# Kernel tuning notes

Hardware: AMD Instinct MI355X
Metric: run time of the kernel (lower is better)

The kernel has to match this reference:

```python
import jax, jax.numpy as jnp
from jax import lax
import numpy as np

B, H, W, C = 2, 128, 128, 256
HEADS, DH = 8, 32
HD = HEADS * DH  # must equal C (pos_emb reshape constraint)


def _lrelu(t):
    return jnp.where(t > 0, t, 0.01 * t)


def _mlp(t, w1, b1, w2):
    # Linear(dim->hd, bias) -> LeakyReLU -> Linear(hd->hd, no bias)
    return _lrelu(t @ w1.T + b1) @ w2.T


def _dwconv(t, w, b):
    # depthwise 3x3, padding 1; t: NCHW, w: (C,1,3,3)
    o = lax.conv_general_dilated(t, w, (1, 1), ((1, 1), (1, 1)),
                                 dimension_numbers=('NCHW', 'OIHW', 'NCHW'),
                                 feature_group_count=t.shape[1])
    return o + b[None, :, None, None]


def setup_inputs():
    key = jax.random.key(0)
    ks = iter(jax.random.split(key, 48))
    def nrm(shape, s=0.02):
        return jax.random.normal(next(ks), shape, jnp.float32) * s
    inp = {
        'x_in': jax.random.normal(next(ks), (B, H, W, C), jnp.float32),
        'y_in': jax.random.normal(next(ks), (B, H, W, C), jnp.float32),
        # fusion_x / fusion_y: two 1x1 convs (stored as (out,in) matrices)
        'fx_w1': nrm((C, 2 * C)), 'fx_b1': jnp.zeros((C,), jnp.float32),
        'fx_w2': nrm((C, C)),     'fx_b2': jnp.zeros((C,), jnp.float32),
        'fy_w1': nrm((C, 2 * C)), 'fy_b1': jnp.zeros((C,), jnp.float32),
        'fy_w2': nrm((C, C)),     'fy_b2': jnp.zeros((C,), jnp.float32),
        # to_q / to_k / to_v: Linear(C->HD,+b) -> LeakyReLU -> Linear(HD->HD, no b)
        'q_w1': nrm((HD, C)), 'q_b1': jnp.zeros((HD,), jnp.float32), 'q_w2': nrm((HD, HD)),
        'k_w1': nrm((HD, C)), 'k_b1': jnp.zeros((HD,), jnp.float32), 'k_w2': nrm((HD, HD)),
        'v_w1': nrm((HD, C)), 'v_b1': jnp.zeros((HD,), jnp.float32), 'v_w2': nrm((HD, HD)),
        'rescale_x': jnp.ones((HEADS, 1, 1), jnp.float32),
        'rescale_y': jnp.ones((HEADS, 1, 1), jnp.float32),
        'px_w': nrm((C, HD)), 'px_b': jnp.zeros((C,), jnp.float32),
        'py_w': nrm((C, HD)), 'py_b': jnp.zeros((C,), jnp.float32),
        # pos_emb: two depthwise 3x3 convs with GELU between
        'pe_w1': nrm((C, 1, 3, 3)), 'pe_b1': jnp.zeros((C,), jnp.float32),
        'pe_w2': nrm((C, 1, 3, 3)), 'pe_b2': jnp.zeros((C,), jnp.float32),
    }
    return inp


def reference(x_in, y_in, fx_w1, fx_b1, fx_w2, fx_b2, fy_w1, fy_b1, fy_w2, fy_b2,
              q_w1, q_b1, q_w2, k_w1, k_b1, k_w2, v_w1, v_b1, v_w2,
              rescale_x, rescale_y, px_w, px_b, py_w, py_b,
              pe_w1, pe_b1, pe_w2, pe_b2):
    b, h, w, c = x_in.shape
    n = h * w

    xy = jnp.concatenate([x_in, y_in], axis=-1)  # (b,h,w,2c)
    fk_x = _lrelu(jnp.einsum('bhwi,oi->bhwo', xy, fx_w1) + fx_b1)
    fk_x = (jnp.einsum('bhwi,oi->bhwo', fk_x, fx_w2) + fx_b2).reshape(b, n, c)
    fk_y = _lrelu(jnp.einsum('bhwi,oi->bhwo', xy, fy_w1) + fy_b1)
    fk_y = (jnp.einsum('bhwi,oi->bhwo', fk_y, fy_w2) + fy_b2).reshape(b, n, c)

    x = x_in.reshape(b, n, c)
    y = y_in.reshape(b, n, c)
    q_inp_x = _mlp(x, q_w1, q_b1, q_w2)
    k_inp_x = _mlp(fk_x, k_w1, k_b1, k_w2)
    v_inp_x = _mlp(x, v_w1, v_b1, v_w2)
    q_inp_y = _mlp(y, q_w1, q_b1, q_w2)
    k_inp_y = _mlp(fk_y, k_w1, k_b1, k_w2)
    v_inp_y = _mlp(y, v_w1, v_b1, v_w2)

    def split_heads(t):  # (b,n,hd) -> (b,heads,d,n)  (already transposed)
        return t.reshape(b, n, HEADS, DH).transpose(0, 2, 3, 1)

    def l2n(t):
        return t / jnp.maximum(jnp.linalg.norm(t, axis=-1, keepdims=True), 1e-12)

    q_x, k_x, v_x = split_heads(q_inp_x), split_heads(k_inp_x), split_heads(v_inp_x)
    q_y, k_y, v_y = split_heads(q_inp_y), split_heads(k_inp_y), split_heads(v_inp_y)
    q_x, k_x, q_y, k_y = l2n(q_x), l2n(k_x), l2n(q_y), l2n(k_y)

    def pos_emb(v_inp):
        t = v_inp.reshape(b, h, w, c).transpose(0, 3, 1, 2)  # NCHW
        t = _dwconv(t, pe_w1, pe_b1)
        t = jax.nn.gelu(t, approximate=False)
        t = _dwconv(t, pe_w2, pe_b2)
        return t.transpose(0, 2, 3, 1)  # NHWC

    # channel (transposed) cross-attention: d x d maps per head
    attn_x = jax.nn.softmax(jnp.einsum('bhdn,bhen->bhde', k_y, q_x) * rescale_x, axis=-1)
    xo = jnp.einsum('bhde,bhen->bhdn', attn_x, v_x).transpose(0, 3, 1, 2).reshape(b, n, HD)
    out_x = (xo @ px_w.T + px_b).reshape(b, h, w, c) + pos_emb(v_inp_x)

    attn_y = jax.nn.softmax(jnp.einsum('bhdn,bhen->bhde', k_x, q_y) * rescale_y, axis=-1)
    yo = jnp.einsum('bhde,bhen->bhdn', attn_y, v_y).transpose(0, 3, 1, 2).reshape(b, n, HD)
    out_y = (yo @ py_w.T + py_b).reshape(b, h, w, c) + pos_emb(v_inp_y)

    return out_x, out_y
```

## Files before the change

### kernel.cpp

```cpp
#include <hip/hip_runtime.h>
#include <hip/hip_bf16.h>

typedef __hip_bfloat16 bf16;
typedef __attribute__((ext_vector_type(8))) short short8;
typedef __attribute__((ext_vector_type(4))) float f32x4;

static __device__ __forceinline__ float bfbits2f(short s) {
    return __uint_as_float(((unsigned int)(unsigned short)s) << 16);
}
static __device__ __forceinline__ bf16 f2bf(float v) { return __float2bfloat16(v); }
static __device__ __forceinline__ short f2bfbits(float f) {
    bf16 h = __float2bfloat16(f);
    return *reinterpret_cast<short*>(&h);
}

struct PrepArgs {
    const float *x, *y; bf16 *xb, *yb;
    const float* wsrc[10]; bf16* wdst[10]; int wblk[10];
    const float *pw1, *pw2; float *t1, *t2;
    float4* zero;
};

__launch_bounds__(256)
__global__ void prep_kernel(PrepArgs a)
{
    int blk = blockIdx.x, tid = threadIdx.x;
    if (blk < 8192) {
        int t = blk * 256 + tid;
        int which = t >> 20;
        size_t i = (size_t)(t & 1048575) * 8;
        const float4* s = (const float4*)((which ? a.y : a.x) + i);
        float4 u = s[0], v = s[1];
        short8 p;
        p[0] = f2bfbits(u.x); p[1] = f2bfbits(u.y); p[2] = f2bfbits(u.z); p[3] = f2bfbits(u.w);
        p[4] = f2bfbits(v.x); p[5] = f2bfbits(v.y); p[6] = f2bfbits(v.z); p[7] = f2bfbits(v.w);
        *(short8*)((which ? a.yb : a.xb) + i) = p;
    } else if (blk < 8960) {
        int b = blk - 8192;
        int ai = 0, base = 0;
        while (ai < 9 && b >= base + a.wblk[ai]) { base += a.wblk[ai]; ++ai; }
        size_t i = ((size_t)(b - base) * 256 + tid) * 4;
        const float4 v = *(const float4*)(a.wsrc[ai] + i);
        bf16* d = a.wdst[ai] + i;
        d[0] = f2bf(v.x); d[1] = f2bf(v.y); d[2] = f2bf(v.z); d[3] = f2bf(v.w);
    } else if (blk < 8978) {
        int t = (blk - 8960) * 256 + tid;
        if (t < 4608) {
            int which = t >= 2304;
            int i = which ? t - 2304 : t;
            int c = i / 9, k = i % 9;
            (which ? a.t2 : a.t1)[k * 256 + c] = (which ? a.pw2 : a.pw1)[i];
        }
    } else {
        int i = (blk - 8978) * 256 + tid;
        a.zero[i] = make_float4(0.f, 0.f, 0.f, 0.f);
    }
}

template<int ROWS>
static __device__ __forceinline__ void stage8(const bf16* __restrict__ g, int ldk,
                                              char* dst, int tid, long r0, int k0)
{
#pragma unroll
    for (int r = 0; r < ROWS / 128; ++r) {
        int row = r * 128 + (tid >> 2);
        int q = (tid & 3) * 16;
        int srcq = q ^ (((row >> 1) & 3) << 4);
        const char* gsrc = (const char*)(g + (size_t)(r0 + row) * ldk + k0) + srcq;
        char* ldst = dst + r * 8192 + ((tid >> 6) << 10);
        __builtin_amdgcn_global_load_lds(
            (const __attribute__((address_space(1))) unsigned int*)gsrc,
            (__attribute__((address_space(3))) unsigned int*)ldst, 16, 0, 0);
    }
}

static __device__ __forceinline__ int h_off2(int r, int c)
{
    return r * 512 + ((c * 2) ^ ((r & 7) << 4));
}

struct MlpArgs {
    const bf16* B1[2]; const float* b1[2];
    const bf16* W2[2]; const float* b2[2];
    bf16* outb[2]; bf16* outT[2]; float* nrm[2];
};

template<int K1, bool CONCAT, bool B2OUT, bool TRANS0>
__launch_bounds__(512, 4)
__global__ void mlp_kernel(const bf16* __restrict__ A0, const bf16* __restrict__ A1,
                           MlpArgs args)
{
    __shared__ __align__(16) char lds[66560];
    int tid = threadIdx.x;
    int lane = tid & 63, wid = tid >> 6;
    int c16 = lane & 15, kg = lane >> 4;
    int wr = wid >> 2, wc = wid & 3;
    int sel = blockIdx.x;
    long m0 = (long)blockIdx.y * 128;
    const bf16* B1p = args.B1[sel];
    const bf16* W2p = args.W2[sel];
    char* Abuf = lds;
    char* Bbuf = lds + 16384;

    f32x4 acc[4][4];
#pragma unroll
    for (int i = 0; i < 4; ++i)
#pragma unroll
        for (int j = 0; j < 4; ++j) acc[i][j] = (f32x4){0.f, 0.f, 0.f, 0.f};

    stage8<128>(A0, 256, Abuf, tid, m0, 0);
    stage8<256>(B1p, K1, Bbuf, tid, 0, 0);

    int kb = kg * 16;
    int offa[4], offb[4];
#pragma unroll
    for (int mi = 0; mi < 4; ++mi) {
        int row = wr * 64 + mi * 16 + c16;
        offa[mi] = row * 64 + (kb ^ (((row >> 1) & 3) << 4));
    }
#pragma unroll
    for (int ni = 0; ni < 4; ++ni) {
        int row = wc * 64 + ni * 16 + c16;
        offb[ni] = row * 64 + (kb ^ (((row >> 1) & 3) << 4));
    }

    constexpr int NT1 = K1 / 32;
#pragma unroll
    for (int kt = 0; kt < NT1; ++kt) {
        __syncthreads();
        int cur = kt & 1;
        if (kt + 1 < NT1) {
            int k0 = (kt + 1) * 32;
            const bf16* As = A0; int kk = k0;
            if (CONCAT && k0 >= 256) { As = A1; kk = k0 - 256; }
            stage8<128>(As, 256, Abuf + (cur ^ 1) * 8192, tid, m0, kk);
            stage8<256>(B1p, K1, Bbuf + (cur ^ 1) * 16384, tid, 0, k0);
        }
        const char* As = Abuf + cur * 8192;
        const char* Bs = Bbuf + cur * 16384;
        short8 af[4], bfr[4];
#pragma unroll
        for (int mi = 0; mi < 4; ++mi) af[mi] = *(const short8*)(As + offa[mi]);
#pragma unroll
        for (int ni = 0; ni < 4; ++ni) bfr[ni] = *(const short8*)(Bs + offb[ni]);
#pragma unroll
        for (int mi = 0; mi < 4; ++mi)
#pragma unroll
            for (int ni = 0; ni < 4; ++ni)
                acc[mi][ni] = __builtin_amdgcn_mfma_f32_16x16x32_bf16(af[mi], bfr[ni], acc[mi][ni], 0, 0, 0);
    }

    int co0 = wid * 32 + c16;
    short8 wf[2][2];
    wf[0][0] = *(const short8*)(W2p + (size_t)co0 * 256 + kg * 8);
    wf[0][1] = *(const short8*)(W2p + (size_t)(co0 + 16) * 256 + kg * 8);

    float bv1[4];
#pragma unroll
    for (int ni = 0; ni < 4; ++ni) bv1[ni] = args.b1[sel][wc * 64 + ni * 16 + c16];
    __syncthreads();
#pragma unroll
    for (int mi = 0; mi < 4; ++mi)
#pragma unroll
        for (int ni = 0; ni < 4; ++ni) {
            int c = wc * 64 + ni * 16 + c16;
#pragma unroll
            for (int j = 0; j < 4; ++j) {
                int r = wr * 64 + mi * 16 + kg * 4 + j;
                float v = acc[mi][ni][j] + bv1[ni];
                v = v > 0.f ? v : 0.01f * v;
                *(bf16*)(lds + h_off2(r, c)) = f2bf(v);
            }
        }
    __syncthreads();

    f32x4 acc2[8][2];
#pragma unroll
    for (int i = 0; i < 8; ++i) {
        acc2[i][0] = (f32x4){0.f, 0.f, 0.f, 0.f};
        acc2[i][1] = (f32x4){0.f, 0.f, 0.f, 0.f};
    }
#pragma unroll
    for (int kc = 0; kc < 8; ++kc) {
        if (kc < 7) {
            wf[(kc + 1) & 1][0] = *(const short8*)(W2p + (size_t)co0 * 256 + (kc + 1) * 32 + kg * 8);
            wf[(kc + 1) & 1][1] = *(const short8*)(W2p + (size_t)(co0 + 16) * 256 + (kc + 1) * 32 + kg * 8);
        }
#pragma unroll
        for (int mi = 0; mi < 8; ++mi) {
            short8 a2 = *(const short8*)(lds + h_off2(mi * 16 + c16, kc * 32 + kg * 8));
            acc2[mi][0] = __builtin_amdgcn_mfma_f32_16x16x32_bf16(a2, wf[kc & 1][0], acc2[mi][0], 0, 0, 0);
            acc2[mi][1] = __builtin_amdgcn_mfma_f32_16x16x32_bf16(a2, wf[kc & 1][1], acc2[mi][1], 0, 0, 0);
        }
    }

    bool trans = TRANS0 && (sel == 0);
    float vsq[2] = {0.f, 0.f};
    __syncthreads();
    if (trans) {
#pragma unroll
        for (int mi = 0; mi < 8; ++mi)
#pragma unroll
            for (int j2 = 0; j2 < 2; ++j2) {
                int col = co0 + j2 * 16;
#pragma unroll
                for (int j = 0; j < 4; ++j) {
                    float v = acc2[mi][j2][j];
                    vsq[j2] += v * v;
                    int row = mi * 16 + kg * 4 + j;
                    *(bf16*)(lds + col * 256 + ((row * 2) ^ ((col & 7) << 4))) = f2bf(v);
                }
            }
    } else {
        const float* b2p = args.b2[sel];
        float bvo[2];
        bvo[0] = B2OUT ? b2p[co0] : 0.f;
        bvo[1] = B2OUT ? b2p[co0 + 16] : 0.f;
#pragma unroll
        for (int mi = 0; mi < 8; ++mi)
#pragma unroll
            for (int j2 = 0; j2 < 2; ++j2) {
                int col = co0 + j2 * 16;
#pragma unroll
                for (int j = 0; j < 4; ++j) {
                    int row = mi * 16 + kg * 4 + j;
                    *(bf16*)(lds + h_off2(row, col)) = f2bf(acc2[mi][j2][j] + bvo[j2]);
                }
            }
    }
    __syncthreads();
    if (trans) {
        bf16* dst = args.outT[sel];
#pragma unroll
        for (int i = 0; i < 8; ++i) {
            int g = i * 512 + tid;
            int col = g >> 4, rc = g & 15;
            short8 vv = *(const short8*)(lds + col * 256 + ((rc ^ (col & 7)) << 4));
            *(short8*)(dst + (size_t)col * 65536 + m0 + rc * 8) = vv;
        }
        float* cs = (float*)(lds + 65536);
        if (tid < 256) cs[tid] = 0.f;
        __syncthreads();
        atomicAdd(&cs[co0], vsq[0]);
        atomicAdd(&cs[co0 + 16], vsq[1]);
        __syncthreads();
        if (tid < 256)
            atomicAdd(args.nrm[sel] + (int)(m0 >> 14) * 256 + tid, cs[tid]);
    } else {
        bf16* dst = args.outb[sel];
#pragma unroll
        for (int i = 0; i < 8; ++i) {
            int g = i * 512 + tid;
            int row = g >> 5, cc = g & 31;
            short8 vv = *(const short8*)(lds + row * 512 + ((cc ^ (row & 7)) << 4));
            *(short8*)(dst + (size_t)(m0 + row) * 256 + cc * 8) = vv;
        }
    }
}

__launch_bounds__(512, 2)
__global__ void projconv_kernel(const bf16* __restrict__ vbuf, const bf16* __restrict__ PW,
                                const bf16* __restrict__ ctmp,
                                const float* __restrict__ px_b, const float* __restrict__ py_b,
                                const float* __restrict__ peT2, const float* __restrict__ pe_b2,
                                float* __restrict__ outf)
{
    __shared__ __align__(16) char lds[76800];
    float* ldsF = (float*)lds;
    float* ldsW = (float*)(lds + 66560);
    float* ldsB = (float*)(lds + 75776);
    int tid = threadIdx.x;
    int lane = tid & 63, wid = tid >> 6;
    int c16 = lane & 15, kg = lane >> 4;
    int wr = wid >> 2, wc = wid & 3;
    long m0 = (long)blockIdx.y * 128;
    int quarter = (int)(m0 >> 14);
    int y = (int)((m0 & 16383) >> 7);
    char* Abuf = lds;
    char* Bbuf = lds + 16384;

    f32x4 acc[4][4];
#pragma unroll
    for (int i = 0; i < 4; ++i)
#pragma unroll
        for (int j = 0; j < 4; ++j) acc[i][j] = (f32x4){0.f, 0.f, 0.f, 0.f};

    const bf16* Bq = PW + (size_t)quarter * 65536;

    stage8<128>(vbuf, 256, Abuf, tid, m0, 0);
    stage8<256>(Bq, 256, Bbuf, tid, 0, 0);

#pragma unroll
    for (int i = 0; i < 5; ++i) {
        int idx = i * 512 + tid;
        if (idx < 2304) ldsW[idx] = peT2[idx];
    }
    if (tid < 256) ldsB[tid] = (quarter < 2 ? px_b : py_b)[tid] + pe_b2[tid];

    int kb = kg * 16;
    int offa[4], offb[4];
#pragma unroll
    for (int mi = 0; mi < 4; ++mi) {
        int row = wr * 64 + mi * 16 + c16;
        offa[mi] = row * 64 + (kb ^ (((row >> 1) & 3) << 4));
    }
#pragma unroll
    for (int ni = 0; ni < 4; ++ni) {
        int row = wc * 64 + ni * 16 + c16;
        offb[ni] = row * 64 + (kb ^ (((row >> 1) & 3) << 4));
    }

#pragma unroll
    for (int kt = 0; kt < 8; ++kt) {
        __syncthreads();
        int cur = kt & 1;
        if (kt + 1 < 8) {
            int k0 = (kt + 1) * 32;
            stage8<128>(vbuf, 256, Abuf + (cur ^ 1) * 8192, tid, m0, k0);
            stage8<256>(Bq, 256, Bbuf + (cur ^ 1) * 16384, tid, 0, k0);
        }
        const char* As = Abuf + cur * 8192;
        const char* Bs = Bbuf + cur * 16384;
        short8 af[4], bfr[4];
#pragma unroll
        for (int mi = 0; mi < 4; ++mi) af[mi] = *(const short8*)(As + offa[mi]);
#pragma unroll
        for (int ni = 0; ni < 4; ++ni) bfr[ni] = *(const short8*)(Bs + offb[ni]);
#pragma unroll
        for (int mi = 0; mi < 4; ++mi)
#pragma unroll
            for (int ni = 0; ni < 4; ++ni)
                acc[mi][ni] = __builtin_amdgcn_mfma_f32_16x16x32_bf16(af[mi], bfr[ni], acc[mi][ni], 0, 0, 0);
    }

    const bf16* cbase = ctmp + (((size_t)quarter << 14) << 8);
#pragma unroll
    for (int hh = 0; hh < 2; ++hh) {
        __syncthreads();
        if (wr == hh) {
#pragma unroll
            for (int mi = 0; mi < 4; ++mi)
#pragma unroll
                for (int ni = 0; ni < 4; ++ni) {
                    int col = wc * 64 + ni * 16 + c16;
#pragma unroll
                    for (int j = 0; j < 4; ++j)
                        ldsF[(mi * 16 + kg * 4 + j) * 260 + col] = acc[mi][ni][j];
                }
        }
        __syncthreads();
#pragma unroll
        for (int pass = 0; pass < 4; ++pass) {
            int idx = pass * 512 + tid;
            int cg = idx & 31, c0 = cg * 8;
            int xl = idx >> 5;
            int x = hh * 64 + xl;
            float a8[8];
#pragma unroll
            for (int j = 0; j < 8; ++j) a8[j] = ldsB[c0 + j];
#pragma unroll
            for (int dy = -1; dy <= 1; ++dy) {
                int yy = y + dy;
                if (yy < 0 || yy > 127) continue;
#pragma unroll
                for (int dx = -1; dx <= 1; ++dx) {
                    int xx = x + dx;
                    if (xx < 0 || xx > 127) continue;
                    short8 v = *(const short8*)(cbase + (size_t)((yy << 7) + xx) * 256 + c0);
                    const float* wt = ldsW + ((dy + 1) * 3 + dx + 1) * 256 + c0;
#pragma unroll
                    for (int j = 0; j < 8; ++j) a8[j] += wt[j] * bfbits2f(v[j]);
                }
            }
            const float* pf = ldsF + xl * 260 + c0;
#pragma unroll
            for (int j = 0; j < 8; ++j) a8[j] += pf[j];
            float4 o0 = make_float4(a8[0], a8[1], a8[2], a8[3]);
            float4 o1 = make_float4(a8[4], a8[5], a8[6], a8[7]);
            float4* op = (float4*)(outf + (size_t)(m0 + x) * 256 + c0);
            op[0] = o0; op[1] = o1;
        }
    }
}

__launch_bounds__(256)
__global__ void convgram_kernel(const bf16* __restrict__ in, const float* __restrict__ wT,
                                const float* __restrict__ bias, bf16* __restrict__ outb,
                                const bf16* __restrict__ qT, const bf16* __restrict__ kT,
                                float* __restrict__ gram)
{
    __shared__ float g[1024];
    int blk = blockIdx.x, tid = threadIdx.x;
    if (blk < 2048) {
        int t = blk * 256 + tid;
        int cg = t & 31;
        int x = (t >> 5) & 127;
        int chunk = (t >> 12) & 31;
        int img = t >> 17;
        int c0 = cg * 8;

        float w[9][8];
#pragma unroll
        for (int k = 0; k < 9; ++k) {
            float4 a = *(const float4*)(wT + k * 256 + c0);
            float4 bq = *(const float4*)(wT + k * 256 + c0 + 4);
            w[k][0] = a.x; w[k][1] = a.y; w[k][2] = a.z; w[k][3] = a.w;
            w[k][4] = bq.x; w[k][5] = bq.y; w[k][6] = bq.z; w[k][7] = bq.w;
        }
        float bs[8];
        {
            float4 a = *(const float4*)(bias + c0);
            float4 bq = *(const float4*)(bias + c0 + 4);
            bs[0] = a.x; bs[1] = a.y; bs[2] = a.z; bs[3] = a.w;
            bs[4] = bq.x; bs[5] = bq.y; bs[6] = bq.z; bs[7] = bq.w;
        }
        const short8 z = (short8){0, 0, 0, 0, 0, 0, 0, 0};
        bool xm = x > 0, xp = x < 127;
        int y0 = chunk * 4;

        for (int yi = 0; yi < 4; ++yi) {
            int y = y0 + yi;
            float acc[8];
#pragma unroll
            for (int j = 0; j < 8; ++j) acc[j] = bs[j];
#pragma unroll
            for (int ky = -1; ky <= 1; ++ky) {
                int yy = y + ky;
                if (yy < 0 || yy > 127) continue;
                const bf16* rp = in + ((((size_t)img << 14) + (yy << 7) + x) << 8) + c0;
                short8 vm = xm ? *(const short8*)(rp - 256) : z;
                short8 vc = *(const short8*)(rp);
                short8 vp = xp ? *(const short8*)(rp + 256) : z;
                int k0 = (ky + 1) * 3;
#pragma unroll
                for (int j = 0; j < 8; ++j) {
                    acc[j] += w[k0 + 0][j] * bfbits2f(vm[j]);
                    acc[j] += w[k0 + 1][j] * bfbits2f(vc[j]);
                    acc[j] += w[k0 + 2][j] * bfbits2f(vp[j]);
                }
            }
            size_t base = ((((size_t)img << 14) + (y << 7) + x) << 8) + c0;
            short8 p;
#pragma unroll
            for (int j = 0; j < 8; ++j) {
                float a = acc[j];
                a = 0.5f * a * (1.0f + erff(a * 0.70710678118654752f));
                p[j] = f2bfbits(a);
            }
            *(short8*)(outb + base) = p;
        }
    } else {
        int bid = blk - 2048;
        int ns = bid & 15, h = (bid >> 4) & 7, b = (bid >> 7) & 1, pair = bid >> 8;
        int lane = tid & 63, w = tid >> 6;
        long krow = pair ? (long)b * 16384 : (long)(32768 + b * 16384);
        long qrow = pair ? (long)(32768 + b * 16384) : (long)b * 16384;
        long nb = (long)ns * 1024 + w * 256 + (lane >> 4) * 8;
        const bf16* Kp = kT + krow + nb;
        const bf16* Qp = qT + qrow + nb;
        int ch = h * 32 + (lane & 15);

        f32x4 acc[2][2];
#pragma unroll
        for (int i = 0; i < 2; ++i)
#pragma unroll
            for (int j = 0; j < 2; ++j) acc[i][j] = (f32x4){0.f, 0.f, 0.f, 0.f};

        for (int it = 0; it < 8; ++it) {
            short8 af[2], bfr[2];
#pragma unroll
            for (int mi = 0; mi < 2; ++mi)
                af[mi] = *(const short8*)(Kp + (size_t)(ch + mi * 16) * 65536 + it * 32);
#pragma unroll
            for (int ni = 0; ni < 2; ++ni)
                bfr[ni] = *(const short8*)(Qp + (size_t)(ch + ni * 16) * 65536 + it * 32);
#pragma unroll
            for (int mi = 0; mi < 2; ++mi)
#pragma unroll
                for (int ni = 0; ni < 2; ++ni)
                    acc[mi][ni] = __builtin_amdgcn_mfma_f32_16x16x32_bf16(af[mi], bfr[ni], acc[mi][ni], 0, 0, 0);
        }

#pragma unroll
        for (int k = 0; k < 4; ++k) g[tid + k * 256] = 0.f;
        __syncthreads();
#pragma unroll
        for (int mi = 0; mi < 2; ++mi)
#pragma unroll
            for (int ni = 0; ni < 2; ++ni) {
                int e = ni * 16 + (lane & 15);
#pragma unroll
                for (int j = 0; j < 4; ++j) {
                    int d = mi * 16 + (lane >> 4) * 4 + j;
                    atomicAdd(&g[d * 32 + e], acc[mi][ni][j]);
                }
            }
        __syncthreads();
        float* gp = gram + ((size_t)((pair * 2 + b) * 8 + h)) * 1024;
#pragma unroll
        for (int k = 0; k < 4; ++k)
            atomicAdd(gp + tid + k * 256, g[tid + k * 256]);
    }
}

__launch_bounds__(256)
__global__ void attn_pw_kernel(const float* __restrict__ gram, const float* __restrict__ norm2,
                               const float* __restrict__ rsx, const float* __restrict__ rsy,
                               const float* __restrict__ pxw, const float* __restrict__ pyw,
                               bf16* __restrict__ PW)
{
    int bid = blockIdx.x;
    int h = bid & 7, b = (bid >> 3) & 1, pair = bid >> 4;
    const float* G = gram + ((size_t)((pair * 2 + b) * 8 + h)) * 1024;
    const float* nk2 = norm2 + (pair ? (4 + b) : (6 + b)) * 256 + h * 32;
    const float* nq2 = norm2 + (pair ? (2 + b) : (0 + b)) * 256 + h * 32;
    float rs = (pair ? rsy : rsx)[h];
    __shared__ float attn[32][32];
    int t = threadIdx.x;
    if (t < 32) {
        int d = t;
        float nk = fmaxf(sqrtf(nk2[d]), 1e-12f);
        float row[32];
        float mx = -3.4e38f;
#pragma unroll
        for (int e = 0; e < 32; ++e) {
            float nq = fmaxf(sqrtf(nq2[e]), 1e-12f);
            float L = G[d * 32 + e] / (nk * nq) * rs;
            row[e] = L;
            mx = fmaxf(mx, L);
        }
        float sum = 0.f;
#pragma unroll
        for (int e = 0; e < 32; ++e) { row[e] = expf(row[e] - mx); sum += row[e]; }
        float inv = 1.0f / sum;
#pragma unroll
        for (int e = 0; e < 32; ++e) attn[d][e] = row[e] * inv;
    }
    __syncthreads();
    const float* pw = pair ? pyw : pxw;
    int o = t;
    float wrow[32];
#pragma unroll
    for (int d2 = 0; d2 < 32; ++d2) wrow[d2] = pw[o * 256 + h * 32 + d2];
    bf16* dst = PW + ((size_t)(pair * 2 + b) * 256 + o) * 256 + h * 32;
#pragma unroll
    for (int e = 0; e < 32; ++e) {
        float sv = 0.f;
#pragma unroll
        for (int d2 = 0; d2 < 32; ++d2) sv += wrow[d2] * attn[d2][e];
        dst[e] = f2bf(sv);
    }
}

extern "C" void kernel_launch(void* const* d_in, const int* in_sizes, int n_in,
                              void* d_out, int out_size, void* d_ws, size_t ws_size,
                              hipStream_t stream)
{
    const float* x_in  = (const float*)d_in[0];
    const float* y_in  = (const float*)d_in[1];
    const float* fx_w1 = (const float*)d_in[2];
    const float* fx_b1 = (const float*)d_in[3];
    const float* fx_w2 = (const float*)d_in[4];
    const float* fx_b2 = (const float*)d_in[5];
    const float* fy_w1 = (const float*)d_in[6];
    const float* fy_b1 = (const float*)d_in[7];
    const float* fy_w2 = (const float*)d_in[8];
    const float* fy_b2 = (const float*)d_in[9];
    const float* q_w1  = (const float*)d_in[10];
    const float* q_b1  = (const float*)d_in[11];
    const float* q_w2  = (const float*)d_in[12];
    const float* k_w1  = (const float*)d_in[13];
    const float* k_b1  = (const float*)d_in[14];
    const float* k_w2  = (const float*)d_in[15];
    const float* v_w1  = (const float*)d_in[16];
    const float* v_b1  = (const float*)d_in[17];
    const float* v_w2  = (const float*)d_in[18];
    const float* rescale_x = (const float*)d_in[19];
    const float* rescale_y = (const float*)d_in[20];
    const float* px_w  = (const float*)d_in[21];
    const float* px_b  = (const float*)d_in[22];
    const float* py_w  = (const float*)d_in[23];
    const float* py_b  = (const float*)d_in[24];
    const float* pe_w1 = (const float*)d_in[25];
    const float* pe_b1 = (const float*)d_in[26];
    const float* pe_w2 = (const float*)d_in[27];
    const float* pe_b2 = (const float*)d_in[28];

    char* ws = (char*)d_ws;
    const size_t NB = 16777216;
    bf16* xbf  = (bf16*)(ws + 0 * NB);
    bf16* ybf  = (bf16*)(ws + 1 * NB);
    bf16* fkx  = (bf16*)(ws + 2 * NB);
    bf16* fky  = (bf16*)(ws + 3 * NB);
    bf16* vbuf = (bf16*)(ws + 4 * NB);
    bf16* qT   = (bf16*)(ws + 6 * NB);
    bf16* kT   = (bf16*)(ws + 8 * NB);
    char* wreg = ws + 10 * NB;
    bf16* w_fx1 = (bf16*)(wreg + 0);
    bf16* w_fx2 = (bf16*)(wreg + 262144);
    bf16* w_fy1 = (bf16*)(wreg + 393216);
    bf16* w_fy2 = (bf16*)(wreg + 655360);
    bf16* w_q1  = (bf16*)(wreg + 786432);
    bf16* w_q2  = (bf16*)(wreg + 917504);
    bf16* w_k1  = (bf16*)(wreg + 1048576);
    bf16* w_k2  = (bf16*)(wreg + 1179648);
    bf16* w_v1  = (bf16*)(wreg + 1310720);
    bf16* w_v2  = (bf16*)(wreg + 1441792);
    float* gram  = (float*)(wreg + 1572864);
    float* norm2 = (float*)(wreg + 1572864 + 131072);
    bf16* PW     = (bf16*)(wreg + 1572864 + 139264);
    float* peT1  = (float*)(wreg + 1572864 + 139264 + 524288);
    float* peT2  = (float*)(wreg + 1572864 + 139264 + 524288 + 9216);
    bf16* ctmp   = fkx;

    float* outx = (float*)d_out;

    PrepArgs pa;
    pa.x = x_in; pa.y = y_in; pa.xb = xbf; pa.yb = ybf;
    const float* ws_src[10] = {fx_w1, fx_w2, fy_w1, fy_w2, q_w1, q_w2, k_w1, k_w2, v_w1, v_w2};
    bf16* ws_dst[10] = {w_fx1, w_fx2, w_fy1, w_fy2, w_q1, w_q2, w_k1, w_k2, w_v1, w_v2};
    int nblk[10] = {128, 64, 128, 64, 64, 64, 64, 64, 64, 64};
    for (int i = 0; i < 10; ++i) { pa.wsrc[i] = ws_src[i]; pa.wdst[i] = ws_dst[i]; pa.wblk[i] = nblk[i]; }
    pa.pw1 = pe_w1; pa.pw2 = pe_w2; pa.t1 = peT1; pa.t2 = peT2;
    pa.zero = (float4*)gram;
    prep_kernel<<<9012, 256, 0, stream>>>(pa);

    MlpArgs fa = {};
    fa.B1[0] = w_fx1; fa.B1[1] = w_fy1; fa.b1[0] = fx_b1; fa.b1[1] = fy_b1;
    fa.W2[0] = w_fx2; fa.W2[1] = w_fy2; fa.b2[0] = fx_b2; fa.b2[1] = fy_b2;
    fa.outb[0] = fkx; fa.outb[1] = fky;
    mlp_kernel<512, true, true, false><<<dim3(2, 256), 512, 0, stream>>>(xbf, ybf, fa);

    MlpArgs qa = {};
    qa.B1[0] = w_q1; qa.B1[1] = w_v1; qa.b1[0] = q_b1; qa.b1[1] = v_b1;
    qa.W2[0] = w_q2; qa.W2[1] = w_v2;
    qa.outT[0] = qT; qa.nrm[0] = norm2;
    qa.outb[1] = vbuf;
    mlp_kernel<256, false, false, true><<<dim3(2, 512), 512, 0, stream>>>(xbf, nullptr, qa);

    MlpArgs ka = {};
    ka.B1[0] = w_k1; ka.b1[0] = k_b1; ka.W2[0] = w_k2;
    ka.outT[0] = kT; ka.nrm[0] = norm2 + 1024;
    mlp_kernel<256, false, false, true><<<dim3(1, 512), 512, 0, stream>>>(fkx, nullptr, ka);

    convgram_kernel<<<2560, 256, 0, stream>>>(vbuf, peT1, pe_b1, ctmp, qT, kT, gram);

    attn_pw_kernel<<<32, 256, 0, stream>>>(gram, norm2, rescale_x, rescale_y, px_w, py_w, PW);

    projconv_kernel<<<dim3(1, 512), 512, 0, stream>>>(vbuf, PW, ctmp, px_b, py_b,
                                                      peT2, pe_b2, outx);
}
```

Baseline: 406.2 us.

## Merge independent MLP launches and co-schedule the k-MLP with the first depthwise conv

```diff
diff --git a/kernel.cpp b/kernel.cpp
--- a/kernel.cpp
+++ b/kernel.cpp
@@ -79,26 +79,17 @@
     return r * 512 + ((c * 2) ^ ((r & 7) << 4));
 }
 
-struct MlpArgs {
-    const bf16* B1[2]; const float* b1[2];
-    const bf16* W2[2]; const float* b2[2];
-    bf16* outb[2]; bf16* outT[2]; float* nrm[2];
-};
-
-template<int K1, bool CONCAT, bool B2OUT, bool TRANS0>
-__launch_bounds__(512, 4)
-__global__ void mlp_kernel(const bf16* __restrict__ A0, const bf16* __restrict__ A1,
-                           MlpArgs args)
-{
-    __shared__ __align__(16) char lds[66560];
-    int tid = threadIdx.x;
+static __device__ __forceinline__ void mlp_body(
+    char* lds, int tid, long m0, int nt1, bool concat,
+    const bf16* __restrict__ A0, const bf16* __restrict__ A1,
+    const bf16* __restrict__ B1p, const float* __restrict__ b1v,
+    const bf16* __restrict__ W2p, const float* __restrict__ b2v,
+    bf16* __restrict__ outb, bf16* __restrict__ outT, float* __restrict__ nrm)
+{
     int lane = tid & 63, wid = tid >> 6;
     int c16 = lane & 15, kg = lane >> 4;
     int wr = wid >> 2, wc = wid & 3;
-    int sel = blockIdx.x;
-    long m0 = (long)blockIdx.y * 128;
-    const bf16* B1p = args.B1[sel];
-    const bf16* W2p = args.W2[sel];
+    int K1 = nt1 * 32;
     char* Abuf = lds;
     char* Bbuf = lds + 16384;
 
@@ -124,15 +115,13 @@
         offb[ni] = row * 64 + (kb ^ (((row >> 1) & 3) << 4));
     }
 
-    constexpr int NT1 = K1 / 32;
-#pragma unroll
-    for (int kt = 0; kt < NT1; ++kt) {
+    for (int kt = 0; kt < nt1; ++kt) {
         __syncthreads();
         int cur = kt & 1;
-        if (kt + 1 < NT1) {
+        if (kt + 1 < nt1) {
             int k0 = (kt + 1) * 32;
             const bf16* As = A0; int kk = k0;
-            if (CONCAT && k0 >= 256) { As = A1; kk = k0 - 256; }
+            if (concat && k0 >= 256) { As = A1; kk = k0 - 256; }
             stage8<128>(As, 256, Abuf + (cur ^ 1) * 8192, tid, m0, kk);
             stage8<256>(B1p, K1, Bbuf + (cur ^ 1) * 16384, tid, 0, k0);
         }
@@ -157,7 +146,7 @@
 
     float bv1[4];
 #pragma unroll
-    for (int ni = 0; ni < 4; ++ni) bv1[ni] = args.b1[sel][wc * 64 + ni * 16 + c16];
+    for (int ni = 0; ni < 4; ++ni) bv1[ni] = b1v[wc * 64 + ni * 16 + c16];
     __syncthreads();
 #pragma unroll
     for (int mi = 0; mi < 4; ++mi)
@@ -194,7 +183,7 @@
         }
     }
 
-    bool trans = TRANS0 && (sel == 0);
+    bool trans = outT != nullptr;
     float vsq[2] = {0.f, 0.f};
     __syncthreads();
     if (trans) {
@@ -212,10 +201,9 @@
                 }
             }
     } else {
-        const float* b2p = args.b2[sel];
         float bvo[2];
-        bvo[0] = B2OUT ? b2p[co0] : 0.f;
-        bvo[1] = B2OUT ? b2p[co0 + 16] : 0.f;
+        bvo[0] = b2v ? b2v[co0] : 0.f;
+        bvo[1] = b2v ? b2v[co0 + 16] : 0.f;
 #pragma unroll
         for (int mi = 0; mi < 8; ++mi)
 #pragma unroll
@@ -230,13 +218,12 @@
     }
     __syncthreads();
     if (trans) {
-        bf16* dst = args.outT[sel];
 #pragma unroll
         for (int i = 0; i < 8; ++i) {
             int g = i * 512 + tid;
             int col = g >> 4, rc = g & 15;
             short8 vv = *(const short8*)(lds + col * 256 + ((rc ^ (col & 7)) << 4));
-            *(short8*)(dst + (size_t)col * 65536 + m0 + rc * 8) = vv;
+            *(short8*)(outT + (size_t)col * 65536 + m0 + rc * 8) = vv;
         }
         float* cs = (float*)(lds + 65536);
         if (tid < 256) cs[tid] = 0.f;
@@ -245,262 +232,168 @@
         atomicAdd(&cs[co0 + 16], vsq[1]);
         __syncthreads();
         if (tid < 256)
-            atomicAdd(args.nrm[sel] + (int)(m0 >> 14) * 256 + tid, cs[tid]);
+            atomicAdd(nrm + (int)(m0 >> 14) * 256 + tid, cs[tid]);
     } else {
-        bf16* dst = args.outb[sel];
 #pragma unroll
         for (int i = 0; i < 8; ++i) {
             int g = i * 512 + tid;
             int row = g >> 5, cc = g & 31;
             short8 vv = *(const short8*)(lds + row * 512 + ((cc ^ (row & 7)) << 4));
-            *(short8*)(dst + (size_t)(m0 + row) * 256 + cc * 8) = vv;
-        }
-    }
-}
-
-__launch_bounds__(512, 2)
-__global__ void projconv_kernel(const bf16* __restrict__ vbuf, const bf16* __restrict__ PW,
-                                const bf16* __restrict__ ctmp,
-                                const float* __restrict__ px_b, const float* __restrict__ py_b,
-                                const float* __restrict__ peT2, const float* __restrict__ pe_b2,
-                                float* __restrict__ outf)
-{
-    __shared__ __align__(16) char lds[76800];
-    float* ldsF = (float*)lds;
-    float* ldsW = (float*)(lds + 66560);
-    float* ldsB = (float*)(lds + 75776);
+            *(short8*)(outb + (size_t)(m0 + row) * 256 + cc * 8) = vv;
+        }
+    }
+}
+
+struct MlpArgs4 {
+    const bf16* A0[4]; const bf16* A1[4];
+    const bf16* B1[4]; const float* b1[4];
+    const bf16* W2[4]; const float* b2[4];
+    bf16* outb[4]; bf16* outT[4]; float* nrm[4];
+    int nt1[4]; int concat[4]; int mblk[4];
+};
+
+__launch_bounds__(512, 4)
+__global__ void fqv_kernel(MlpArgs4 a)
+{
+    __shared__ __align__(16) char lds[66560];
+    int sel = blockIdx.x;
+    if ((int)blockIdx.y >= a.mblk[sel]) return;
+    long m0 = (long)blockIdx.y * 128;
+    mlp_body(lds, threadIdx.x, m0, a.nt1[sel], a.concat[sel] != 0,
+             a.A0[sel], a.A1[sel], a.B1[sel], a.b1[sel], a.W2[sel], a.b2[sel],
+             a.outb[sel], a.outT[sel], a.nrm[sel]);
+}
+
+__launch_bounds__(512, 4)
+__global__ void kconv_kernel(const bf16* __restrict__ fk,
+                             const bf16* __restrict__ w_k1, const float* __restrict__ k_b1,
+                             const bf16* __restrict__ w_k2,
+                             bf16* __restrict__ kT, float* __restrict__ nrm,
+                             const bf16* __restrict__ vin, const float* __restrict__ wT,
+                             const float* __restrict__ cbias, bf16* __restrict__ ctmp)
+{
+    __shared__ __align__(16) char lds[66560];
+    int blk = blockIdx.x;
+    if (blk < 512) {
+        mlp_body(lds, threadIdx.x, (long)blk * 128, 8, false,
+                 fk, nullptr, w_k1, k_b1, w_k2, nullptr, nullptr, kT, nrm);
+        return;
+    }
+    int t = (blk - 512) * 512 + threadIdx.x;
+    int cg = t & 31;
+    int x = (t >> 5) & 127;
+    int chunk = (t >> 12) & 31;
+    int img = t >> 17;
+    int c0 = cg * 8;
+
+    float w[9][8];
+#pragma unroll
+    for (int k = 0; k < 9; ++k) {
+        float4 aq = *(const float4*)(wT + k * 256 + c0);
+        float4 bq = *(const float4*)(wT + k * 256 + c0 + 4);
+        w[k][0] = aq.x; w[k][1] = aq.y; w[k][2] = aq.z; w[k][3] = aq.w;
+        w[k][4] = bq.x; w[k][5] = bq.y; w[k][6] = bq.z; w[k][7] = bq.w;
+    }
+    float bs[8];
+    {
+        float4 aq = *(const float4*)(cbias + c0);
+        float4 bq = *(const float4*)(cbias + c0 + 4);
+        bs[0] = aq.x; bs[1] = aq.y; bs[2] = aq.z; bs[3] = aq.w;
+        bs[4] = bq.x; bs[5] = bq.y; bs[6] = bq.z; bs[7] = bq.w;
+    }
+    const short8 z = (short8){0, 0, 0, 0, 0, 0, 0, 0};
+    bool xm = x > 0, xp = x < 127;
+    int y0 = chunk * 4;
+
+    for (int yi = 0; yi < 4; ++yi) {
+        int y = y0 + yi;
+        float acc[8];
+#pragma unroll
+        for (int j = 0; j < 8; ++j) acc[j] = bs[j];
+#pragma unroll
+        for (int ky = -1; ky <= 1; ++ky) {
+            int yy = y + ky;
+            if (yy < 0 || yy > 127) continue;
+            const bf16* rp = vin + ((((size_t)img << 14) + (yy << 7) + x) << 8) + c0;
+            short8 vm = xm ? *(const short8*)(rp - 256) : z;
+            short8 vc = *(const short8*)(rp);
+            short8 vp = xp ? *(const short8*)(rp + 256) : z;
+            int k0 = (ky + 1) * 3;
+#pragma unroll
+            for (int j = 0; j < 8; ++j) {
+                acc[j] += w[k0 + 0][j] * bfbits2f(vm[j]);
+                acc[j] += w[k0 + 1][j] * bfbits2f(vc[j]);
+                acc[j] += w[k0 + 2][j] * bfbits2f(vp[j]);
+            }
+        }
+        size_t base = ((((size_t)img << 14) + (y << 7) + x) << 8) + c0;
+        short8 p;
+#pragma unroll
+        for (int j = 0; j < 8; ++j) {
+            float aa = acc[j];
+            aa = 0.5f * aa * (1.0f + erff(aa * 0.70710678118654752f));
+            p[j] = f2bfbits(aa);
+        }
+        *(short8*)(ctmp + base) = p;
+    }
+}
+
+__launch_bounds__(256)
+__global__ void gram_mfma_kernel(const bf16* __restrict__ qT, const bf16* __restrict__ kT,
+                                 float* __restrict__ gram)
+{
+    __shared__ float g[1024];
+    int bid = blockIdx.x;
+    int ns = bid & 15, h = (bid >> 4) & 7, b = (bid >> 7) & 1, pair = bid >> 8;
     int tid = threadIdx.x;
-    int lane = tid & 63, wid = tid >> 6;
-    int c16 = lane & 15, kg = lane >> 4;
-    int wr = wid >> 2, wc = wid & 3;
-    long m0 = (long)blockIdx.y * 128;
-    int quarter = (int)(m0 >> 14);
-    int y = (int)((m0 & 16383) >> 7);
-    char* Abuf = lds;
-    char* Bbuf = lds + 16384;
-
-    f32x4 acc[4][4];
-#pragma unroll
-    for (int i = 0; i < 4; ++i)
-#pragma unroll
-        for (int j = 0; j < 4; ++j) acc[i][j] = (f32x4){0.f, 0.f, 0.f, 0.f};
-
-    const bf16* Bq = PW + (size_t)quarter * 65536;
-
-    stage8<128>(vbuf, 256, Abuf, tid, m0, 0);
-    stage8<256>(Bq, 256, Bbuf, tid, 0, 0);
-
-#pragma unroll
-    for (int i = 0; i < 5; ++i) {
-        int idx = i * 512 + tid;
-        if (idx < 2304) ldsW[idx] = peT2[idx];
-    }
-    if (tid < 256) ldsB[tid] = (quarter < 2 ? px_b : py_b)[tid] + pe_b2[tid];
-
-    int kb = kg * 16;
-    int offa[4], offb[4];
-#pragma unroll
-    for (int mi = 0; mi < 4; ++mi) {
-        int row = wr * 64 + mi * 16 + c16;
-        offa[mi] = row * 64 + (kb ^ (((row >> 1) & 3) << 4));
-    }
-#pragma unroll
-    for (int ni = 0; ni < 4; ++ni) {
-        int row = wc * 64 + ni * 16 + c16;
-        offb[ni] = row * 64 + (kb ^ (((row >> 1) & 3) << 4));
-    }
-
-#pragma unroll
-    for (int kt = 0; kt < 8; ++kt) {
-        __syncthreads();
-        int cur = kt & 1;
-        if (kt + 1 < 8) {
-            int k0 = (kt + 1) * 32;
-            stage8<128>(vbuf, 256, Abuf + (cur ^ 1) * 8192, tid, m0, k0);
-            stage8<256>(Bq, 256, Bbuf + (cur ^ 1) * 16384, tid, 0, k0);
-        }
-        const char* As = Abuf + cur * 8192;
-        const char* Bs = Bbuf + cur * 16384;
-        short8 af[4], bfr[4];
-#pragma unroll
-        for (int mi = 0; mi < 4; ++mi) af[mi] = *(const short8*)(As + offa[mi]);
-#pragma unroll
-        for (int ni = 0; ni < 4; ++ni) bfr[ni] = *(const short8*)(Bs + offb[ni]);
-#pragma unroll
-        for (int mi = 0; mi < 4; ++mi)
-#pragma unroll
-            for (int ni = 0; ni < 4; ++ni)
+    int lane = tid & 63, w = tid >> 6;
+    long krow = pair ? (long)b * 16384 : (long)(32768 + b * 16384);
+    long qrow = pair ? (long)(32768 + b * 16384) : (long)b * 16384;
+    long nb = (long)ns * 1024 + w * 256 + (lane >> 4) * 8;
+    const bf16* Kp = kT + krow + nb;
+    const bf16* Qp = qT + qrow + nb;
+    int ch = h * 32 + (lane & 15);
+
+    f32x4 acc[2][2];
+#pragma unroll
+    for (int i = 0; i < 2; ++i)
+#pragma unroll
+        for (int j = 0; j < 2; ++j) acc[i][j] = (f32x4){0.f, 0.f, 0.f, 0.f};
+
+    for (int it = 0; it < 8; ++it) {
+        short8 af[2], bfr[2];
+#pragma unroll
+        for (int mi = 0; mi < 2; ++mi)
+            af[mi] = *(const short8*)(Kp + (size_t)(ch + mi * 16) * 65536 + it * 32);
+#pragma unroll
+        for (int ni = 0; ni < 2; ++ni)
+            bfr[ni] = *(const short8*)(Qp + (size_t)(ch + ni * 16) * 65536 + it * 32);
+#pragma unroll
+        for (int mi = 0; mi < 2; ++mi)
+#pragma unroll
+            for (int ni = 0; ni < 2; ++ni)
                 acc[mi][ni] = __builtin_amdgcn_mfma_f32_16x16x32_bf16(af[mi], bfr[ni], acc[mi][ni], 0, 0, 0);
     }
 
-    const bf16* cbase = ctmp + (((size_t)quarter << 14) << 8);
-#pragma unroll
-    for (int hh = 0; hh < 2; ++hh) {
-        __syncthreads();
-        if (wr == hh) {
-#pragma unroll
-            for (int mi = 0; mi < 4; ++mi)
-#pragma unroll
-                for (int ni = 0; ni < 4; ++ni) {
-                    int col = wc * 64 + ni * 16 + c16;
-#pragma unroll
-                    for (int j = 0; j < 4; ++j)
-                        ldsF[(mi * 16 + kg * 4 + j) * 260 + col] = acc[mi][ni][j];
-                }
-        }
-        __syncthreads();
-#pragma unroll
-        for (int pass = 0; pass < 4; ++pass) {
-            int idx = pass * 512 + tid;
-            int cg = idx & 31, c0 = cg * 8;
-            int xl = idx >> 5;
-            int x = hh * 64 + xl;
-            float a8[8];
-#pragma unroll
-            for (int j = 0; j < 8; ++j) a8[j] = ldsB[c0 + j];
-#pragma unroll
-            for (int dy = -1; dy <= 1; ++dy) {
-                int yy = y + dy;
-                if (yy < 0 || yy > 127) continue;
-#pragma unroll
-                for (int dx = -1; dx <= 1; ++dx) {
-                    int xx = x + dx;
-                    if (xx < 0 || xx > 127) continue;
-                    short8 v = *(const short8*)(cbase + (size_t)((yy << 7) + xx) * 256 + c0);
-                    const float* wt = ldsW + ((dy + 1) * 3 + dx + 1) * 256 + c0;
-#pragma unroll
-                    for (int j = 0; j < 8; ++j) a8[j] += wt[j] * bfbits2f(v[j]);
-                }
+#pragma unroll
+    for (int k = 0; k < 4; ++k) g[tid + k * 256] = 0.f;
+    __syncthreads();
+#pragma unroll
+    for (int mi = 0; mi < 2; ++mi)
+#pragma unroll
+        for (int ni = 0; ni < 2; ++ni) {
+            int e = ni * 16 + (lane & 15);
+#pragma unroll
+            for (int j = 0; j < 4; ++j) {
+                int d = mi * 16 + (lane >> 4) * 4 + j;
+                atomicAdd(&g[d * 32 + e], acc[mi][ni][j]);
             }
-            const float* pf = ldsF + xl * 260 + c0;
-#pragma unroll
-            for (int j = 0; j < 8; ++j) a8[j] += pf[j];
-            float4 o0 = make_float4(a8[0], a8[1], a8[2], a8[3]);
-            float4 o1 = make_float4(a8[4], a8[5], a8[6], a8[7]);
-            float4* op = (float4*)(outf + (size_t)(m0 + x) * 256 + c0);
-            op[0] = o0; op[1] = o1;
-        }
-    }
-}
-
-__launch_bounds__(256)
-__global__ void convgram_kernel(const bf16* __restrict__ in, const float* __restrict__ wT,
-                                const float* __restrict__ bias, bf16* __restrict__ outb,
-                                const bf16* __restrict__ qT, const bf16* __restrict__ kT,
-                                float* __restrict__ gram)
-{
-    __shared__ float g[1024];
-    int blk = blockIdx.x, tid = threadIdx.x;
-    if (blk < 2048) {
-        int t = blk * 256 + tid;
-        int cg = t & 31;
-        int x = (t >> 5) & 127;
-        int chunk = (t >> 12) & 31;
-        int img = t >> 17;
-        int c0 = cg * 8;
-
-        float w[9][8];
-#pragma unroll
-        for (int k = 0; k < 9; ++k) {
-            float4 a = *(const float4*)(wT + k * 256 + c0);
-            float4 bq = *(const float4*)(wT + k * 256 + c0 + 4);
-            w[k][0] = a.x; w[k][1] = a.y; w[k][2] = a.z; w[k][3] = a.w;
-            w[k][4] = bq.x; w[k][5] = bq.y; w[k][6] = bq.z; w[k][7] = bq.w;
-        }
-        float bs[8];
-        {
-            float4 a = *(const float4*)(bias + c0);
-            float4 bq = *(const float4*)(bias + c0 + 4);
-            bs[0] = a.x; bs[1] = a.y; bs[2] = a.z; bs[3] = a.w;
-            bs[4] = bq.x; bs[5] = bq.y; bs[6] = bq.z; bs[7] = bq.w;
-        }
-        const short8 z = (short8){0, 0, 0, 0, 0, 0, 0, 0};
-        bool xm = x > 0, xp = x < 127;
-        int y0 = chunk * 4;
-
-        for (int yi = 0; yi < 4; ++yi) {
-            int y = y0 + yi;
-            float acc[8];
-#pragma unroll
-            for (int j = 0; j < 8; ++j) acc[j] = bs[j];
-#pragma unroll
-            for (int ky = -1; ky <= 1; ++ky) {
-                int yy = y + ky;
-                if (yy < 0 || yy > 127) continue;
-                const bf16* rp = in + ((((size_t)img << 14) + (yy << 7) + x) << 8) + c0;
-                short8 vm = xm ? *(const short8*)(rp - 256) : z;
-                short8 vc = *(const short8*)(rp);
-                short8 vp = xp ? *(const short8*)(rp + 256) : z;
-                int k0 = (ky + 1) * 3;
-#pragma unroll
-                for (int j = 0; j < 8; ++j) {
-                    acc[j] += w[k0 + 0][j] * bfbits2f(vm[j]);
-                    acc[j] += w[k0 + 1][j] * bfbits2f(vc[j]);
-                    acc[j] += w[k0 + 2][j] * bfbits2f(vp[j]);
-                }
-            }
-            size_t base = ((((size_t)img << 14) + (y << 7) + x) << 8) + c0;
-            short8 p;
-#pragma unroll
-            for (int j = 0; j < 8; ++j) {
-                float a = acc[j];
-                a = 0.5f * a * (1.0f + erff(a * 0.70710678118654752f));
-                p[j] = f2bfbits(a);
-            }
-            *(short8*)(outb + base) = p;
-        }
-    } else {
-        int bid = blk - 2048;
-        int ns = bid & 15, h = (bid >> 4) & 7, b = (bid >> 7) & 1, pair = bid >> 8;
-        int lane = tid & 63, w = tid >> 6;
-        long krow = pair ? (long)b * 16384 : (long)(32768 + b * 16384);
-        long qrow = pair ? (long)(32768 + b * 16384) : (long)b * 16384;
-        long nb = (long)ns * 1024 + w * 256 + (lane >> 4) * 8;
-        const bf16* Kp = kT + krow + nb;
-        const bf16* Qp = qT + qrow + nb;
-        int ch = h * 32 + (lane & 15);
-
-        f32x4 acc[2][2];
-#pragma unroll
-        for (int i = 0; i < 2; ++i)
-#pragma unroll
-            for (int j = 0; j < 2; ++j) acc[i][j] = (f32x4){0.f, 0.f, 0.f, 0.f};
-
-        for (int it = 0; it < 8; ++it) {
-            short8 af[2], bfr[2];
-#pragma unroll
-            for (int mi = 0; mi < 2; ++mi)
-                af[mi] = *(const short8*)(Kp + (size_t)(ch + mi * 16) * 65536 + it * 32);
-#pragma unroll
-            for (int ni = 0; ni < 2; ++ni)
-                bfr[ni] = *(const short8*)(Qp + (size_t)(ch + ni * 16) * 65536 + it * 32);
-#pragma unroll
-            for (int mi = 0; mi < 2; ++mi)
-#pragma unroll
-                for (int ni = 0; ni < 2; ++ni)
-                    acc[mi][ni] = __builtin_amdgcn_mfma_f32_16x16x32_bf16(af[mi], bfr[ni], acc[mi][ni], 0, 0, 0);
-        }
-
-#pragma unroll
-        for (int k = 0; k < 4; ++k) g[tid + k * 256] = 0.f;
-        __syncthreads();
-#pragma unroll
-        for (int mi = 0; mi < 2; ++mi)
-#pragma unroll
-            for (int ni = 0; ni < 2; ++ni) {
-                int e = ni * 16 + (lane & 15);
-#pragma unroll
-                for (int j = 0; j < 4; ++j) {
-                    int d = mi * 16 + (lane >> 4) * 4 + j;
-                    atomicAdd(&g[d * 32 + e], acc[mi][ni][j]);
-                }
-            }
-        __syncthreads();
-        float* gp = gram + ((size_t)((pair * 2 + b) * 8 + h)) * 1024;
-#pragma unroll
-        for (int k = 0; k < 4; ++k)
-            atomicAdd(gp + tid + k * 256, g[tid + k * 256]);
-    }
+        }
+    __syncthreads();
+    float* gp = gram + ((size_t)((pair * 2 + b) * 8 + h)) * 1024;
+#pragma unroll
+    for (int k = 0; k < 4; ++k)
+        atomicAdd(gp + tid + k * 256, g[tid + k * 256]);
 }
 
 __launch_bounds__(256)
@@ -549,6 +442,133 @@
 #pragma unroll
         for (int d2 = 0; d2 < 32; ++d2) sv += wrow[d2] * attn[d2][e];
         dst[e] = f2bf(sv);
+    }
+}
+
+__launch_bounds__(512, 6)
+__global__ void projconv_kernel(const bf16* __restrict__ vbuf, const bf16* __restrict__ PW,
+                                const bf16* __restrict__ ctmp,
+                                const float* __restrict__ px_b, const float* __restrict__ py_b,
+                                const float* __restrict__ peT2, const float* __restrict__ pe_b2,
+                                float* __restrict__ outf)
+{
+    __shared__ __align__(16) char lds[49152];
+    float* ldsF = (float*)lds;
+    float* ldsW = (float*)(lds + 33792);
+    float* ldsB = (float*)(lds + 43008);
+    int tid = threadIdx.x;
+    int lane = tid & 63, wid = tid >> 6;
+    int c16 = lane & 15, kg = lane >> 4;
+    int wr = wid >> 2, wc = wid & 3;
+    long m0 = (long)blockIdx.y * 128;
+    int quarter = (int)(m0 >> 14);
+    int y = (int)((m0 & 16383) >> 7);
+    char* Abuf = lds;
+    char* Bbuf = lds + 16384;
+
+    f32x4 acc[4][4];
+#pragma unroll
+    for (int i = 0; i < 4; ++i)
+#pragma unroll
+        for (int j = 0; j < 4; ++j) acc[i][j] = (f32x4){0.f, 0.f, 0.f, 0.f};
+
+    const bf16* Bq = PW + (size_t)quarter * 65536;
+
+    stage8<128>(vbuf, 256, Abuf, tid, m0, 0);
+    stage8<256>(Bq, 256, Bbuf, tid, 0, 0);
+
+    int kb = kg * 16;
+    int offa[4], offb[4];
+#pragma unroll
+    for (int mi = 0; mi < 4; ++mi) {
+        int row = wr * 64 + mi * 16 + c16;
+        offa[mi] = row * 64 + (kb ^ (((row >> 1) & 3) << 4));
+    }
+#pragma unroll
+    for (int ni = 0; ni < 4; ++ni) {
+        int row = wc * 64 + ni * 16 + c16;
+        offb[ni] = row * 64 + (kb ^ (((row >> 1) & 3) << 4));
+    }
+
+#pragma unroll
+    for (int kt = 0; kt < 8; ++kt) {
+        __syncthreads();
+        int cur = kt & 1;
+        if (kt + 1 < 8) {
+            int k0 = (kt + 1) * 32;
+            stage8<128>(vbuf, 256, Abuf + (cur ^ 1) * 8192, tid, m0, k0);
+            stage8<256>(Bq, 256, Bbuf + (cur ^ 1) * 16384, tid, 0, k0);
+        }
+        const char* As = Abuf + cur * 8192;
+        const char* Bs = Bbuf + cur * 16384;
+        short8 af[4], bfr[4];
+#pragma unroll
+        for (int mi = 0; mi < 4; ++mi) af[mi] = *(const short8*)(As + offa[mi]);
+#pragma unroll
+        for (int ni = 0; ni < 4; ++ni) bfr[ni] = *(const short8*)(Bs + offb[ni]);
+#pragma unroll
+        for (int mi = 0; mi < 4; ++mi)
+#pragma unroll
+            for (int ni = 0; ni < 4; ++ni)
+                acc[mi][ni] = __builtin_amdgcn_mfma_f32_16x16x32_bf16(af[mi], bfr[ni], acc[mi][ni], 0, 0, 0);
+    }
+    __syncthreads();
+
+#pragma unroll
+    for (int i = 0; i < 5; ++i) {
+        int idx = i * 512 + tid;
+        if (idx < 2304) ldsW[idx] = peT2[idx];
+    }
+    if (tid < 256) ldsB[tid] = (quarter < 2 ? px_b : py_b)[tid] + pe_b2[tid];
+
+    const bf16* cbase = ctmp + (((size_t)quarter << 14) << 8);
+#pragma unroll
+    for (int hh = 0; hh < 4; ++hh) {
+        int mb = (hh & 1) * 2;
+        if (wr == (hh >> 1)) {
+#pragma unroll
+            for (int mi2 = 0; mi2 < 2; ++mi2)
+#pragma unroll
+                for (int ni = 0; ni < 4; ++ni) {
+                    int col = wc * 64 + ni * 16 + c16;
+#pragma unroll
+                    for (int j = 0; j < 4; ++j)
+                        ldsF[(mi2 * 16 + kg * 4 + j) * 264 + col] = acc[mb + mi2][ni][j];
+                }
+        }
+        __syncthreads();
+#pragma unroll
+        for (int pass = 0; pass < 2; ++pass) {
+            int idx = pass * 512 + tid;
+            int cg = idx & 31, c0 = cg * 8;
+            int xl = idx >> 5;
+            int x = hh * 32 + xl;
+            float a8[8];
+#pragma unroll
+            for (int j = 0; j < 8; ++j) a8[j] = ldsB[c0 + j];
+#pragma unroll
+            for (int dy = -1; dy <= 1; ++dy) {
+                int yy = y + dy;
+                if (yy < 0 || yy > 127) continue;
+#pragma unroll
+                for (int dx = -1; dx <= 1; ++dx) {
+                    int xx = x + dx;
+                    if (xx < 0 || xx > 127) continue;
+                    short8 v = *(const short8*)(cbase + (size_t)((yy << 7) + xx) * 256 + c0);
+                    const float* wt = ldsW + ((dy + 1) * 3 + dx + 1) * 256 + c0;
+#pragma unroll
+                    for (int j = 0; j < 8; ++j) a8[j] += wt[j] * bfbits2f(v[j]);
+                }
+            }
+            const float* pf = ldsF + xl * 264 + c0;
+            float4 p0 = *(const float4*)(pf);
+            float4 p1 = *(const float4*)(pf + 4);
+            float4 o0 = make_float4(a8[0] + p0.x, a8[1] + p0.y, a8[2] + p0.z, a8[3] + p0.w);
+            float4 o1 = make_float4(a8[4] + p1.x, a8[5] + p1.y, a8[6] + p1.z, a8[7] + p1.w);
+            float4* op = (float4*)(outf + (size_t)(m0 + x) * 256 + c0);
+            op[0] = o0; op[1] = o1;
+        }
+        __syncthreads();
     }
 }
 
@@ -611,7 +631,7 @@
     bf16* PW     = (bf16*)(wreg + 1572864 + 139264);
     float* peT1  = (float*)(wreg + 1572864 + 139264 + 524288);
     float* peT2  = (float*)(wreg + 1572864 + 139264 + 524288 + 9216);
-    bf16* ctmp   = fkx;
+    bf16* ctmp   = xbf;
 
     float* outx = (float*)d_out;
 
@@ -625,25 +645,25 @@
     pa.zero = (float4*)gram;
     prep_kernel<<<9012, 256, 0, stream>>>(pa);
 
-    MlpArgs fa = {};
-    fa.B1[0] = w_fx1; fa.B1[1] = w_fy1; fa.b1[0] = fx_b1; fa.b1[1] = fy_b1;
-    fa.W2[0] = w_fx2; fa.W2[1] = w_fy2; fa.b2[0] = fx_b2; fa.b2[1] = fy_b2;
-    fa.outb[0] = fkx; fa.outb[1] = fky;
-    mlp_kernel<512, true, true, false><<<dim3(2, 256), 512, 0, stream>>>(xbf, ybf, fa);
-
-    MlpArgs qa = {};
-    qa.B1[0] = w_q1; qa.B1[1] = w_v1; qa.b1[0] = q_b1; qa.b1[1] = v_b1;
-    qa.W2[0] = w_q2; qa.W2[1] = w_v2;
-    qa.outT[0] = qT; qa.nrm[0] = norm2;
-    qa.outb[1] = vbuf;
-    mlp_kernel<256, false, false, true><<<dim3(2, 512), 512, 0, stream>>>(xbf, nullptr, qa);
-
-    MlpArgs ka = {};
-    ka.B1[0] = w_k1; ka.b1[0] = k_b1; ka.W2[0] = w_k2;
-    ka.outT[0] = kT; ka.nrm[0] = norm2 + 1024;
-    mlp_kernel<256, false, false, true><<<dim3(1, 512), 512, 0, stream>>>(fkx, nullptr, ka);
-
-    convgram_kernel<<<2560, 256, 0, stream>>>(vbuf, peT1, pe_b1, ctmp, qT, kT, gram);
+    MlpArgs4 fa = {};
+    fa.A0[0] = xbf; fa.A1[0] = ybf; fa.B1[0] = w_fx1; fa.b1[0] = fx_b1;
+    fa.W2[0] = w_fx2; fa.b2[0] = fx_b2; fa.outb[0] = fkx;
+    fa.nt1[0] = 16; fa.concat[0] = 1; fa.mblk[0] = 256;
+    fa.A0[1] = xbf; fa.A1[1] = ybf; fa.B1[1] = w_fy1; fa.b1[1] = fy_b1;
+    fa.W2[1] = w_fy2; fa.b2[1] = fy_b2; fa.outb[1] = fky;
+    fa.nt1[1] = 16; fa.concat[1] = 1; fa.mblk[1] = 256;
+    fa.A0[2] = xbf; fa.B1[2] = w_q1; fa.b1[2] = q_b1; fa.W2[2] = w_q2;
+    fa.outT[2] = qT; fa.nrm[2] = norm2;
+    fa.nt1[2] = 8; fa.concat[2] = 0; fa.mblk[2] = 512;
+    fa.A0[3] = xbf; fa.B1[3] = w_v1; fa.b1[3] = v_b1; fa.W2[3] = w_v2;
+    fa.outb[3] = vbuf;
+    fa.nt1[3] = 8; fa.concat[3] = 0; fa.mblk[3] = 512;
+    fqv_kernel<<<dim3(4, 512), 512, 0, stream>>>(fa);
+
+    kconv_kernel<<<1536, 512, 0, stream>>>(fkx, w_k1, k_b1, w_k2, kT, norm2 + 1024,
+                                           vbuf, peT1, pe_b1, ctmp);
+
+    gram_mfma_kernel<<<512, 256, 0, stream>>>(qT, kT, gram);
 
     attn_pw_kernel<<<32, 256, 0, stream>>>(gram, norm2, rescale_x, rescale_y, px_w, py_w, PW);
 
```

After: 475.6 us. 17.1% more time.
